# Kernel tuning notes

Measured on AMD Instinct MI355X. Metric: run time of the kernel, lower is better.

The kernel has to match this reference:

```python
import jax, jax.numpy as jnp
import numpy as np

D_MODEL = 1024
D_FF = 4096
NUM_EXPERTS = 8
TOP_K = 2
LB_COEF = 0.01
Z_COEF = 0.001
EPS_LN = 1e-5


def setup_inputs() -> dict:
    key = jax.random.key(0)
    ks = jax.random.split(key, 8)
    B, L = 4, 2048
    s_in = 1.0 / np.sqrt(D_MODEL)
    s_ff = 1.0 / np.sqrt(D_FF)
    return {
        "x": jax.random.normal(ks[0], (B, L, D_MODEL), dtype=jnp.float32),
        "gate_w": jax.random.normal(ks[1], (NUM_EXPERTS, D_MODEL), dtype=jnp.float32) * s_in,
        "ln_g": jnp.ones((D_MODEL,), dtype=jnp.float32),
        "ln_b": jnp.zeros((D_MODEL,), dtype=jnp.float32),
        "w1": jax.random.normal(ks[2], (NUM_EXPERTS, D_MODEL, D_FF), dtype=jnp.float32) * s_in,
        "b1": jnp.zeros((NUM_EXPERTS, D_FF), dtype=jnp.float32),
        "w2": jax.random.normal(ks[3], (NUM_EXPERTS, D_FF, D_MODEL), dtype=jnp.float32) * s_ff,
        "b2": jnp.zeros((NUM_EXPERTS, D_MODEL), dtype=jnp.float32),
    }


def reference(x, gate_w, ln_g, ln_b, w1, b1, w2, b2):
    B, L, D = x.shape
    xf = x.reshape(-1, D)  # [T, D]

    # LayerNorm
    mu = jnp.mean(xf, axis=-1, keepdims=True)
    var = jnp.mean((xf - mu) ** 2, axis=-1, keepdims=True)
    x_norm = (xf - mu) * jax.lax.rsqrt(var + EPS_LN) * ln_g + ln_b

    # Router (eval mode: no noise)
    logits = jnp.clip(x_norm @ gate_w.T, -10.0, 10.0)  # [T, E]
    z_loss = jnp.mean(jax.nn.logsumexp(logits, axis=-1) ** 2) * Z_COEF
    probs = jax.nn.softmax(logits, axis=-1)

    gw, idx = jax.lax.top_k(probs, TOP_K)  # [T, K]
    gw = gw / (jnp.sum(gw, axis=-1, keepdims=True) + 1e-8)

    # Load-balancing aux loss uses top-1 assignment
    top1_mask = jax.nn.one_hot(idx[:, 0], NUM_EXPERTS, dtype=jnp.float32)
    fraction_routed = jnp.mean(top1_mask, axis=0)
    mean_prob = jnp.mean(probs, axis=0)
    aux_loss = NUM_EXPERTS * jnp.sum(fraction_routed * mean_prob) * LB_COEF
    total_aux = aux_loss + z_loss

    # Combine weights [T, E]: sum over k of gate weight where routed to e
    combine = jnp.einsum("tk,tke->te", gw, jax.nn.one_hot(idx, NUM_EXPERTS, dtype=gw.dtype))

    # Dense per-expert FFN (Expert: Linear -> GELU -> Linear), combined by weights
    out = jnp.zeros_like(xf)
    for e in range(NUM_EXPERTS):
        h = jax.nn.gelu(x_norm @ w1[e] + b1[e], approximate=False)
        y = h @ w2[e] + b2[e]
        out = out + combine[:, e:e + 1] * y

    return x + out.reshape(B, L, D), total_aux
```

## Files before the change

kernel.cpp:

```cpp
#include <hip/hip_runtime.h>
#include <math.h>

typedef __bf16 bf16_t;
typedef bf16_t bf16x8 __attribute__((ext_vector_type(8)));
typedef bf16_t bf16x4 __attribute__((ext_vector_type(4)));
typedef float  f32x4  __attribute__((ext_vector_type(4)));

#define T_TOK 8192
#define DM 1024
#define DF 4096
#define NE 8
#define NP 16384

__device__ __forceinline__ f32x4 mfma_bf16(bf16x8 a, bf16x8 b, f32x4 c) {
  return __builtin_amdgcn_mfma_f32_16x16x32_bf16(a, b, c, 0, 0, 0);
}

__device__ __forceinline__ void gload16(const void* g, void* l) {
  __builtin_amdgcn_global_load_lds((const __attribute__((address_space(1))) void*)g,
                                   (__attribute__((address_space(3))) void*)l, 16, 0, 0);
}

__device__ __forceinline__ float erf_fast(float x) {
  float ax = fabsf(x);
  float t = 1.f / (1.f + 0.3275911f * ax);
  float p = t * (0.254829592f + t * (-0.284496736f + t * (1.421413741f +
            t * (-1.453152027f + t * 1.061405429f))));
  float r = 1.f - p * __expf(-ax * ax);
  return copysignf(r, x);
}

__device__ __forceinline__ unsigned swz_off(int row, int ch) {
  return (unsigned)(((row >> 1) << 7) + (((((row & 1) << 2) | ch) ^ ((row >> 1) & 7)) << 4));
}


__global__ __launch_bounds__(256) void k_router(
    const float* __restrict__ x, const float* __restrict__ gate_w,
    const float* __restrict__ ln_g, const float* __restrict__ ln_b,
    float* __restrict__ out, bf16_t* __restrict__ xn,
    int* __restrict__ eidx, float* __restrict__ gts, int* __restrict__ meta)
{
  int* cnt1 = meta;
  int* cnt2 = meta + 8;
  float* probsum = (float*)(meta + 32);
  float* zsum    = (float*)(meta + 40);

  __shared__ float sprob[8];
  __shared__ float sz;
  __shared__ int sc1[8], sc2[8];
  if (threadIdx.x < 8) { sprob[threadIdx.x] = 0.f; sc1[threadIdx.x] = 0; sc2[threadIdx.x] = 0; }
  if (threadIdx.x == 8) sz = 0.f;
  __syncthreads();

  int lane = threadIdx.x & 63, wv = threadIdx.x >> 6;
  int t = blockIdx.x * 4 + wv;
  const float* xt = x + (size_t)t * DM;

  float4 v[4];
  float s1 = 0.f, s2 = 0.f;
  #pragma unroll
  for (int c = 0; c < 4; ++c) {
    v[c] = *(const float4*)(xt + c * 256 + lane * 4);
    s1 += v[c].x + v[c].y + v[c].z + v[c].w;
    s2 += v[c].x * v[c].x + v[c].y * v[c].y + v[c].z * v[c].z + v[c].w * v[c].w;
  }
  #pragma unroll
  for (int o = 32; o > 0; o >>= 1) { s1 += __shfl_xor(s1, o, 64); s2 += __shfl_xor(s2, o, 64); }
  float mu = s1 * (1.f / DM);
  float var = s2 * (1.f / DM) - mu * mu;
  float rstd = rsqrtf(var + 1e-5f);

  float xv[16];
  #pragma unroll
  for (int c = 0; c < 4; ++c) {
    int d = c * 256 + lane * 4;
    float4 g4 = *(const float4*)(ln_g + d);
    float4 b4 = *(const float4*)(ln_b + d);
    xv[c*4+0] = (v[c].x - mu) * rstd * g4.x + b4.x;
    xv[c*4+1] = (v[c].y - mu) * rstd * g4.y + b4.y;
    xv[c*4+2] = (v[c].z - mu) * rstd * g4.z + b4.z;
    xv[c*4+3] = (v[c].w - mu) * rstd * g4.w + b4.w;
    *(float4*)(out + (size_t)t * DM + d) = v[c];
    bf16x4 pk = { (bf16_t)xv[c*4+0], (bf16_t)xv[c*4+1], (bf16_t)xv[c*4+2], (bf16_t)xv[c*4+3] };
    *(bf16x4*)(xn + (size_t)t * DM + d) = pk;
  }

  float lg[8];
  #pragma unroll
  for (int e = 0; e < 8; ++e) {
    float p = 0.f;
    #pragma unroll
    for (int c = 0; c < 4; ++c) {
      int d = c * 256 + lane * 4;
      float4 g4 = *(const float4*)(gate_w + e * DM + d);
      p += xv[c*4+0] * g4.x + xv[c*4+1] * g4.y + xv[c*4+2] * g4.z + xv[c*4+3] * g4.w;
    }
    #pragma unroll
    for (int o = 32; o > 0; o >>= 1) p += __shfl_xor(p, o, 64);
    lg[e] = p;
  }

  if (lane == 0) {
    float m = -1e30f;
    #pragma unroll
    for (int e = 0; e < 8; ++e) { lg[e] = fminf(fmaxf(lg[e], -10.f), 10.f); m = fmaxf(m, lg[e]); }
    float pr[8]; float se = 0.f;
    #pragma unroll
    for (int e = 0; e < 8; ++e) { pr[e] = expf(lg[e] - m); se += pr[e]; }
    float inv = 1.f / se;
    #pragma unroll
    for (int e = 0; e < 8; ++e) pr[e] *= inv;
    float lse = m + logf(se);

    int e0 = 0; float p0 = pr[0];
    #pragma unroll
    for (int e = 1; e < 8; ++e) if (pr[e] > p0) { p0 = pr[e]; e0 = e; }
    int e1 = -1; float p1 = -1.f;
    #pragma unroll
    for (int e = 0; e < 8; ++e) if (e != e0 && pr[e] > p1) { p1 = pr[e]; e1 = e; }
    float s = p0 + p1 + 1e-8f;
    eidx[t*2]   = e0; eidx[t*2+1] = e1;
    gts[t*2]    = p0 / s; gts[t*2+1] = p1 / s;

    atomicAdd(&sc1[e0], 1);
    atomicAdd(&sc2[e0], 1);
    atomicAdd(&sc2[e1], 1);
    #pragma unroll
    for (int e = 0; e < 8; ++e) atomicAdd(&sprob[e], pr[e]);
    atomicAdd(&sz, lse * lse);
  }
  __syncthreads();
  if (threadIdx.x < 8) {
    if (sc1[threadIdx.x]) atomicAdd(&cnt1[threadIdx.x], sc1[threadIdx.x]);
    if (sc2[threadIdx.x]) atomicAdd(&cnt2[threadIdx.x], sc2[threadIdx.x]);
    atomicAdd(&probsum[threadIdx.x], sprob[threadIdx.x]);
  }
  if (threadIdx.x == 8) atomicAdd(zsum, sz);
}

__global__ __launch_bounds__(256) void k_convT2(
    const float* __restrict__ w1, bf16_t* __restrict__ w1t,
    const float* __restrict__ w2, bf16_t* __restrict__ w2t)
{
  int bid = blockIdx.x;
  const float* s; bf16_t* d; int R, C, c0, r0;
  if (bid < 8192) {
    int e = bid >> 10, rem = bid & 1023;
    R = DM; C = DF;
    s = w1 + (size_t)e * R * C; d = w1t + (size_t)e * R * C;
    c0 = (rem & 63) * 64; r0 = (rem >> 6) * 64;
  } else {
    int e = (bid - 8192) >> 10, rem = (bid - 8192) & 1023;
    R = DF; C = DM;
    s = w2 + (size_t)e * R * C; d = w2t + (size_t)e * R * C;
    c0 = (rem & 15) * 64; r0 = (rem >> 4) * 64;
  }

  __shared__ float tile[64][65];
  int t = threadIdx.x;
  #pragma unroll
  for (int i = 0; i < 4; ++i) {
    int idx = i * 256 + t;
    int r = idx >> 4, c4 = (idx & 15) * 4;
    float4 v = *(const float4*)(s + (size_t)(r0 + r) * C + c0 + c4);
    tile[r][c4]   = v.x; tile[r][c4+1] = v.y;
    tile[r][c4+2] = v.z; tile[r][c4+3] = v.w;
  }
  __syncthreads();
  #pragma unroll
  for (int i = 0; i < 2; ++i) {
    int idx = i * 256 + t;
    int c = idx >> 3, r8 = (idx & 7) * 8;
    bf16x8 pk;
    #pragma unroll
    for (int k = 0; k < 8; ++k) pk[k] = (bf16_t)tile[r8 + k][c];
    *(bf16x8*)(d + (size_t)(c0 + c) * R + r0 + r8) = pk;
  }
}

__global__ void k_finalize(int* __restrict__ meta, float* __restrict__ aux_out) {
  if (threadIdx.x == 0 && blockIdx.x == 0) {
    int acc = 0;
    for (int e = 0; e < 8; ++e) { meta[24 + e] = acc; acc += meta[8 + e]; }
    const float* probsum = (const float*)(meta + 32);
    const float* zsum    = (const float*)(meta + 40);
    float s = 0.f;
    for (int e = 0; e < 8; ++e)
      s += ((float)meta[e] * (1.f / 8192.f)) * (probsum[e] * (1.f / 8192.f));
    aux_out[0] = 8.f * s * 0.01f + (zsum[0] * (1.f / 8192.f)) * 0.001f;
  }
}

__global__ __launch_bounds__(256) void k_assign(
    const int* __restrict__ eidx, float* __restrict__ gts,
    int* __restrict__ meta, int* __restrict__ list, float* __restrict__ gl,
    int* __restrict__ t2s)
{
  int t = blockIdx.x * 256 + threadIdx.x;
  int* cursor = meta + 16;
  const int* off = meta + 24;
  #pragma unroll
  for (int k = 0; k < 2; ++k) {
    int e = eidx[t*2 + k];
    float g = gts[t*2 + k];
    int pos = atomicAdd(&cursor[e], 1);
    int slot = off[e] + pos;
    list[slot] = t;
    gl[slot] = g;
    t2s[t*2 + k] = slot;
  }
}


#define PBAR do { __builtin_amdgcn_sched_barrier(0); __builtin_amdgcn_s_barrier(); \
                  __builtin_amdgcn_sched_barrier(0); } while (0)
#define VWAIT10 do { __builtin_amdgcn_sched_barrier(0); \
  asm volatile("s_waitcnt vmcnt(10)" ::: "memory"); \
  __builtin_amdgcn_sched_barrier(0); } while (0)
#define VWAIT0 do { __builtin_amdgcn_sched_barrier(0); \
  asm volatile("s_waitcnt vmcnt(0)" ::: "memory"); \
  __builtin_amdgcn_sched_barrier(0); } while (0)

#define STG_A(T, KS, P) do { \
  gload16(sAq[0] + (T)*64 + (KS)*32, smem + (P)*65536 + (KS)*16384 + dq[0]); \
  gload16(sAq[1] + (T)*64 + (KS)*32, smem + (P)*65536 + (KS)*16384 + dq[1]); } while (0)
#define STG_B(T, KS, P) do { \
  gload16(sBq[0] + (T)*64 + (KS)*32, smem + (P)*65536 + 32768 + (KS)*16384 + dq[0]); \
  gload16(sBq[1] + (T)*64 + (KS)*32, smem + (P)*65536 + 32768 + (KS)*16384 + dq[1]); } while (0)
#define LDA(P, KS) do { _Pragma("unroll") for (int i_ = 0; i_ < 8; ++i_) \
  afr[i_] = *(const bf16x8*)(smem + (P)*65536 + (KS)*16384 + a_off[i_]); } while (0)
#define LDB(P, KS, NH) do { \
  bfr0 = *(const bf16x8*)(smem + (P)*65536 + 32768 + (KS)*16384 + b_off[(NH)*2+0]); \
  bfr1 = *(const bf16x8*)(smem + (P)*65536 + 32768 + (KS)*16384 + b_off[(NH)*2+1]); } while (0)
#define FMA(NH) do { __builtin_amdgcn_s_setprio(1); \
  _Pragma("unroll") for (int i_ = 0; i_ < 8; ++i_) { \
    acc[i_][(NH)*2+0] = mfma_bf16(afr[i_], bfr0, acc[i_][(NH)*2+0]); \
    acc[i_][(NH)*2+1] = mfma_bf16(afr[i_], bfr1, acc[i_][(NH)*2+1]); } \
  __builtin_amdgcn_s_setprio(0); } while (0)

#define TILE_MAIN(T, P) do { \
  LDA(P,0); LDB(P,0,0); STG_B((T)+1, 1, (P)^1); PBAR; FMA(0); PBAR; \
  LDB(P,0,1); STG_A((T)+2, 0, P); VWAIT10; PBAR; FMA(1); PBAR; \
  LDA(P,1); LDB(P,1,0); STG_B((T)+2, 0, P); PBAR; FMA(0); PBAR; \
  LDB(P,1,1); STG_A((T)+2, 1, P); VWAIT10; PBAR; FMA(1); PBAR; } while (0)

#define GEMM_PIPE(NT) do { \
  STG_A(0,0,0); STG_B(0,0,0); STG_A(0,1,0); STG_B(0,1,0); \
  STG_A(1,0,1); STG_B(1,0,1); STG_A(1,1,1); \
  VWAIT10; PBAR; \
  for (int t_ = 0; t_ < (NT) - 2; t_ += 2) { TILE_MAIN(t_, 0); TILE_MAIN(t_ + 1, 1); } \
   \
  LDA(0,0); LDB(0,0,0); STG_B((NT)-1, 1, 1); PBAR; FMA(0); PBAR; \
  LDB(0,0,1); VWAIT0; PBAR; FMA(1); PBAR; \
  LDA(0,1); LDB(0,1,0); PBAR; FMA(0); PBAR; \
  LDB(0,1,1); PBAR; FMA(1); PBAR; \
   \
  LDA(1,0); LDB(1,0,0); PBAR; FMA(0); PBAR; \
  LDB(1,0,1); PBAR; FMA(1); PBAR; \
  LDA(1,1); LDB(1,1,0); PBAR; FMA(0); PBAR; \
  LDB(1,1,1); PBAR; FMA(1); \
} while (0)

__global__ __launch_bounds__(512, 1) void k_ffn1(
    const bf16_t* __restrict__ xn, const bf16_t* __restrict__ w1t,
    const float* __restrict__ b1, bf16_t* __restrict__ H,
    const int* __restrict__ list, const int* __restrict__ meta)
{
  extern __shared__ char smem[];
  int e = blockIdx.z;
  int cnt = meta[8 + e];
  int m0 = blockIdx.y * 256;
  if (m0 >= cnt) return;
  int offe = meta[24 + e];
  int n0 = blockIdx.x * 256;

  int tid = threadIdx.x, lane = tid & 63, wv = tid >> 6;
  int wm = wv >> 2, wn = wv & 3;

  const bf16_t* sAq[2]; const bf16_t* sBq[2];
  unsigned dq[2];
  #pragma unroll
  for (int i = 0; i < 2; ++i) {
    int s = i * 512 + tid;
    int line = s >> 3, u = s & 7, w = u ^ (line & 7);
    int row = (line << 1) | (w >> 2), ch = w & 3;
    int mrow = min(m0 + row, cnt - 1);
    int token = list[offe + mrow];
    sAq[i] = xn + (size_t)token * DM + ch * 8;
    sBq[i] = w1t + ((size_t)e * DF + n0 + row) * DM + ch * 8;
    dq[i] = (unsigned)(i * 8192 + wv * 1024);
  }

  unsigned a_off[8], b_off[4];
  #pragma unroll
  for (int i = 0; i < 8; ++i) a_off[i] = swz_off(wm * 128 + i * 16 + (lane & 15), lane >> 4);
  #pragma unroll
  for (int j = 0; j < 4; ++j)
    b_off[j] = swz_off(wn * 64 + (j >> 1) * 32 + (j & 1) * 16 + (lane & 15), lane >> 4);

  f32x4 acc[8][4];
  #pragma unroll
  for (int i = 0; i < 8; ++i)
    #pragma unroll
    for (int j = 0; j < 4; ++j)
      acc[i][j] = (f32x4){0.f, 0.f, 0.f, 0.f};
  bf16x8 afr[8], bfr0, bfr1;

  GEMM_PIPE(DM / 64);

  int rq = (lane >> 4) << 2;
  int cb = n0 + wn * 64 + (lane & 15);
  #pragma unroll
  for (int i = 0; i < 8; ++i) {
    #pragma unroll
    for (int q = 0; q < 4; ++q) {
      int mg = m0 + wm * 128 + i * 16 + rq + q;
      if (mg < cnt) {
        size_t hrow = (size_t)(offe + mg) * DF;
        #pragma unroll
        for (int j = 0; j < 4; ++j) {
          int col = cb + (j >> 1) * 32 + (j & 1) * 16;
          float hv = acc[i][j][q] + b1[e * DF + col];
          hv = 0.5f * hv * (1.f + erf_fast(hv * 0.70710678118f));
          H[hrow + col] = (bf16_t)hv;
        }
      }
    }
  }
}

__global__ __launch_bounds__(512, 1) void k_ffn2(
    const bf16_t* __restrict__ H, const bf16_t* __restrict__ w2t,
    const float* __restrict__ b2, bf16_t* __restrict__ Y,
    const int* __restrict__ meta)
{
  extern __shared__ char smem[];
  int e = blockIdx.z;
  int cnt = meta[8 + e];
  int m0 = blockIdx.y * 256;
  if (m0 >= cnt) return;
  int offe = meta[24 + e];
  int n0 = blockIdx.x * 256;

  int tid = threadIdx.x, lane = tid & 63, wv = tid >> 6;
  int wm = wv >> 2, wn = wv & 3;

  const bf16_t* sAq[2]; const bf16_t* sBq[2];
  unsigned dq[2];
  #pragma unroll
  for (int i = 0; i < 2; ++i) {
    int s = i * 512 + tid;
    int line = s >> 3, u = s & 7, w = u ^ (line & 7);
    int row = (line << 1) | (w >> 2), ch = w & 3;
    int mrow = min(m0 + row, cnt - 1);
    sAq[i] = H + (size_t)(offe + mrow) * DF + ch * 8;
    sBq[i] = w2t + ((size_t)e * DM + n0 + row) * DF + ch * 8;
    dq[i] = (unsigned)(i * 8192 + wv * 1024);
  }

  unsigned a_off[8], b_off[4];
  #pragma unroll
  for (int i = 0; i < 8; ++i) a_off[i] = swz_off(wm * 128 + i * 16 + (lane & 15), lane >> 4);
  #pragma unroll
  for (int j = 0; j < 4; ++j)
    b_off[j] = swz_off(wn * 64 + (j >> 1) * 32 + (j & 1) * 16 + (lane & 15), lane >> 4);

  f32x4 acc[8][4];
  #pragma unroll
  for (int i = 0; i < 8; ++i)
    #pragma unroll
    for (int j = 0; j < 4; ++j)
      acc[i][j] = (f32x4){0.f, 0.f, 0.f, 0.f};
  bf16x8 afr[8], bfr0, bfr1;

  GEMM_PIPE(DF / 64);

  int rq = (lane >> 4) << 2;
  int cb = n0 + wn * 64 + (lane & 15);
  #pragma unroll
  for (int i = 0; i < 8; ++i) {
    #pragma unroll
    for (int q = 0; q < 4; ++q) {
      int mg = m0 + wm * 128 + i * 16 + rq + q;
      if (mg < cnt) {
        size_t yrow = (size_t)(offe + mg) * DM;
        #pragma unroll
        for (int j = 0; j < 4; ++j) {
          int col = cb + (j >> 1) * 32 + (j & 1) * 16;
          Y[yrow + col] = (bf16_t)(acc[i][j][q] + b2[e * DM + col]);
        }
      }
    }
  }
}

__global__ __launch_bounds__(256) void k_combine(
    const bf16_t* __restrict__ Y, const int* __restrict__ t2s,
    const float* __restrict__ gl, float* __restrict__ out)
{
  int lane = threadIdx.x & 63, wv = threadIdx.x >> 6;
  int t = blockIdx.x * 4 + wv;
  int s0 = t2s[t*2], s1 = t2s[t*2 + 1];
  float g0 = gl[s0], g1 = gl[s1];
  const bf16_t* y0 = Y + (size_t)s0 * DM;
  const bf16_t* y1 = Y + (size_t)s1 * DM;
  float* o = out + (size_t)t * DM;
  #pragma unroll
  for (int c = 0; c < 4; ++c) {
    int d = c * 256 + lane * 4;
    float4 r  = *(const float4*)(o + d);
    bf16x4 a = *(const bf16x4*)(y0 + d);
    bf16x4 b = *(const bf16x4*)(y1 + d);
    r.x += g0 * (float)a[0] + g1 * (float)b[0];
    r.y += g0 * (float)a[1] + g1 * (float)b[1];
    r.z += g0 * (float)a[2] + g1 * (float)b[2];
    r.w += g0 * (float)a[3] + g1 * (float)b[3];
    *(float4*)(o + d) = r;
  }
}

extern "C" void kernel_launch(void* const* d_in, const int* in_sizes, int n_in,
                              void* d_out, int out_size, void* d_ws, size_t ws_size,
                              hipStream_t stream) {
  const float* x      = (const float*)d_in[0];
  const float* gate_w = (const float*)d_in[1];
  const float* ln_g   = (const float*)d_in[2];
  const float* ln_b   = (const float*)d_in[3];
  const float* w1     = (const float*)d_in[4];
  const float* b1     = (const float*)d_in[5];
  const float* w2     = (const float*)d_in[6];
  const float* b2     = (const float*)d_in[7];
  float* out = (float*)d_out;

  char* ws = (char*)d_ws;
  bf16_t* xn   = (bf16_t*)(ws);
  bf16_t* w1t  = (bf16_t*)(ws + 16777216ull);
  bf16_t* Y    = (bf16_t*)(ws + 16777216ull);
  bf16_t* w2t  = (bf16_t*)(ws + 83886080ull);
  bf16_t* H    = (bf16_t*)(ws + 150994944ull);
  int*    list = (int*)   (ws + 285212672ull);
  float*  gl   = (float*) (ws + 285278208ull);
  int*    eidx = (int*)   (ws + 285343744ull);
  float*  gts  = (float*) (ws + 285409280ull);
  int*    t2s  = (int*)   (ws + 285409280ull);
  int*    meta = (int*)   (ws + 285474816ull);

  hipFuncSetAttribute((const void*)k_ffn1, hipFuncAttributeMaxDynamicSharedMemorySize, 131072);
  hipFuncSetAttribute((const void*)k_ffn2, hipFuncAttributeMaxDynamicSharedMemorySize, 131072);

  hipMemsetAsync(meta, 0, 256, stream);
  k_router<<<T_TOK / 4, 256, 0, stream>>>(x, gate_w, ln_g, ln_b, out, xn, eidx, gts, meta);
  k_convT2<<<16384, 256, 0, stream>>>(w1, w1t, w2, w2t);
  k_finalize<<<1, 1, 0, stream>>>(meta, out + (size_t)T_TOK * DM);
  k_assign<<<T_TOK / 256, 256, 0, stream>>>(eidx, gts, meta, list, gl, t2s);
  k_ffn1<<<dim3(DF / 256, 32, NE), 512, 131072, stream>>>(xn, w1t, b1, H, list, meta);
  k_ffn2<<<dim3(DM / 256, 32, NE), 512, 131072, stream>>>(H, w2t, b2, Y, meta);
  k_combine<<<T_TOK / 4, 256, 0, stream>>>(Y, t2s, gl, out);
}
```

Before: 663.1 us.

## Restructure GEMM pipeline to one barrier per quarter-step with double A fragments

Rewrites the LDS-staged MFMA pipeline in both expert FFN kernels. The old scheme put two s_barriers around each MFMA burst and prefetched two tiles ahead. The new one issues each quarter-tile global-to-LDS load for the next tile, then waits with a finer vmcnt and a single barrier before the LDS reads and MFMAs. Separate A fragment registers for the two k-halves let the compiler overlap LDS reads with MFMA execution. The aim is to halve barrier count and reduce stalls, at the cost of a shallower prefetch (one tile ahead) and more VGPR pressure, which may expose global load latency.

```diff
diff --git a/kernel.cpp b/kernel.cpp
--- a/kernel.cpp
+++ b/kernel.cpp
@@ -213,14 +213,8 @@
 }
 
 
-#define PBAR do { __builtin_amdgcn_sched_barrier(0); __builtin_amdgcn_s_barrier(); \
-                  __builtin_amdgcn_sched_barrier(0); } while (0)
-#define VWAIT10 do { __builtin_amdgcn_sched_barrier(0); \
-  asm volatile("s_waitcnt vmcnt(10)" ::: "memory"); \
-  __builtin_amdgcn_sched_barrier(0); } while (0)
-#define VWAIT0 do { __builtin_amdgcn_sched_barrier(0); \
-  asm volatile("s_waitcnt vmcnt(0)" ::: "memory"); \
-  __builtin_amdgcn_sched_barrier(0); } while (0)
+#define VW(N) asm volatile("s_waitcnt vmcnt(" #N ")" ::: "memory")
+#define BARSB do { __builtin_amdgcn_s_barrier(); __builtin_amdgcn_sched_barrier(0); } while (0)
 
 #define STG_A(T, KS, P) do { \
   gload16(sAq[0] + (T)*64 + (KS)*32, smem + (P)*65536 + (KS)*16384 + dq[0]); \
@@ -228,38 +222,45 @@
 #define STG_B(T, KS, P) do { \
   gload16(sBq[0] + (T)*64 + (KS)*32, smem + (P)*65536 + 32768 + (KS)*16384 + dq[0]); \
   gload16(sBq[1] + (T)*64 + (KS)*32, smem + (P)*65536 + 32768 + (KS)*16384 + dq[1]); } while (0)
-#define LDA(P, KS) do { _Pragma("unroll") for (int i_ = 0; i_ < 8; ++i_) \
-  afr[i_] = *(const bf16x8*)(smem + (P)*65536 + (KS)*16384 + a_off[i_]); } while (0)
-#define LDB(P, KS, NH) do { \
-  bfr0 = *(const bf16x8*)(smem + (P)*65536 + 32768 + (KS)*16384 + b_off[(NH)*2+0]); \
-  bfr1 = *(const bf16x8*)(smem + (P)*65536 + 32768 + (KS)*16384 + b_off[(NH)*2+1]); } while (0)
-#define FMA(NH) do { __builtin_amdgcn_s_setprio(1); \
+
+#define LDA_(AF, P, KS) do { _Pragma("unroll") for (int i_ = 0; i_ < 8; ++i_) \
+  AF[i_] = *(const bf16x8*)(smem + (P)*65536 + (KS)*16384 + a_off[i_]); } while (0)
+#define LDBA(P, KS) do { \
+  bfrA0 = *(const bf16x8*)(smem + (P)*65536 + 32768 + (KS)*16384 + b_off[0]); \
+  bfrA1 = *(const bf16x8*)(smem + (P)*65536 + 32768 + (KS)*16384 + b_off[1]); } while (0)
+#define LDBB(P, KS) do { \
+  bfrB0 = *(const bf16x8*)(smem + (P)*65536 + 32768 + (KS)*16384 + b_off[2]); \
+  bfrB1 = *(const bf16x8*)(smem + (P)*65536 + 32768 + (KS)*16384 + b_off[3]); } while (0)
+
+#define FMAQ(AF, B0, B1, NH) do { __builtin_amdgcn_s_setprio(1); \
   _Pragma("unroll") for (int i_ = 0; i_ < 8; ++i_) { \
-    acc[i_][(NH)*2+0] = mfma_bf16(afr[i_], bfr0, acc[i_][(NH)*2+0]); \
-    acc[i_][(NH)*2+1] = mfma_bf16(afr[i_], bfr1, acc[i_][(NH)*2+1]); } \
+    acc[i_][(NH)*2+0] = mfma_bf16(AF[i_], B0, acc[i_][(NH)*2+0]); \
+    acc[i_][(NH)*2+1] = mfma_bf16(AF[i_], B1, acc[i_][(NH)*2+1]); } \
   __builtin_amdgcn_s_setprio(0); } while (0)
 
-#define TILE_MAIN(T, P) do { \
-  LDA(P,0); LDB(P,0,0); STG_B((T)+1, 1, (P)^1); PBAR; FMA(0); PBAR; \
-  LDB(P,0,1); STG_A((T)+2, 0, P); VWAIT10; PBAR; FMA(1); PBAR; \
-  LDA(P,1); LDB(P,1,0); STG_B((T)+2, 0, P); PBAR; FMA(0); PBAR; \
-  LDB(P,1,1); STG_A((T)+2, 1, P); VWAIT10; PBAR; FMA(1); PBAR; } while (0)
+#define TILE(T, P) do { \
+  STG_A((T)+1, 0, (P)^1); VW(6); BARSB; \
+  LDA_(afr0, P, 0); LDBA(P, 0); FMAQ(afr0, bfrA0, bfrA1, 0); \
+  STG_B((T)+1, 0, (P)^1); VW(8); BARSB; \
+  LDBB(P, 0); FMAQ(afr0, bfrB0, bfrB1, 1); \
+  STG_A((T)+1, 1, (P)^1); VW(6); BARSB; \
+  LDA_(afr1, P, 1); LDBA(P, 1); FMAQ(afr1, bfrA0, bfrA1, 0); \
+  STG_B((T)+1, 1, (P)^1); VW(8); BARSB; \
+  LDBB(P, 1); FMAQ(afr1, bfrB0, bfrB1, 1); \
+} while (0)
+
+#define TAIL(P) do { \
+  VW(4); BARSB; LDA_(afr0, P, 0); LDBA(P, 0); FMAQ(afr0, bfrA0, bfrA1, 0); \
+  VW(4); BARSB; LDBB(P, 0); FMAQ(afr0, bfrB0, bfrB1, 1); \
+  VW(0); BARSB; LDA_(afr1, P, 1); LDBA(P, 1); FMAQ(afr1, bfrA0, bfrA1, 0); \
+  VW(0); BARSB; LDBB(P, 1); FMAQ(afr1, bfrB0, bfrB1, 1); \
+} while (0)
 
 #define GEMM_PIPE(NT) do { \
-  STG_A(0,0,0); STG_B(0,0,0); STG_A(0,1,0); STG_B(0,1,0); \
-  STG_A(1,0,1); STG_B(1,0,1); STG_A(1,1,1); \
-  VWAIT10; PBAR; \
-  for (int t_ = 0; t_ < (NT) - 2; t_ += 2) { TILE_MAIN(t_, 0); TILE_MAIN(t_ + 1, 1); } \
-   \
-  LDA(0,0); LDB(0,0,0); STG_B((NT)-1, 1, 1); PBAR; FMA(0); PBAR; \
-  LDB(0,0,1); VWAIT0; PBAR; FMA(1); PBAR; \
-  LDA(0,1); LDB(0,1,0); PBAR; FMA(0); PBAR; \
-  LDB(0,1,1); PBAR; FMA(1); PBAR; \
-   \
-  LDA(1,0); LDB(1,0,0); PBAR; FMA(0); PBAR; \
-  LDB(1,0,1); PBAR; FMA(1); PBAR; \
-  LDA(1,1); LDB(1,1,0); PBAR; FMA(0); PBAR; \
-  LDB(1,1,1); PBAR; FMA(1); \
+  STG_A(0, 0, 0); STG_B(0, 0, 0); STG_A(0, 1, 0); STG_B(0, 1, 0); \
+  for (int t_ = 0; t_ + 2 < (NT); t_ += 2) { TILE(t_, 0); TILE(t_ + 1, 1); } \
+  TILE((NT) - 2, 0); \
+  TAIL(1); \
 } while (0)
 
 __global__ __launch_bounds__(512, 1) void k_ffn1(
@@ -305,7 +306,7 @@
     #pragma unroll
     for (int j = 0; j < 4; ++j)
       acc[i][j] = (f32x4){0.f, 0.f, 0.f, 0.f};
-  bf16x8 afr[8], bfr0, bfr1;
+  bf16x8 afr0[8], afr1[8], bfrA0, bfrA1, bfrB0, bfrB1;
 
   GEMM_PIPE(DM / 64);
 
@@ -372,7 +373,7 @@
     #pragma unroll
     for (int j = 0; j < 4; ++j)
       acc[i][j] = (f32x4){0.f, 0.f, 0.f, 0.f};
-  bf16x8 afr[8], bfr0, bfr1;
+  bf16x8 afr0[8], afr1[8], bfrA0, bfrA1, bfrB0, bfrB1;
 
   GEMM_PIPE(DF / 64);
 
```

After: 648.7 us. -2.2%, faster.
